# Optimization experiments

Hardware: AMD Instinct MI355X
Metric: run time of the kernel (lower is better)

The kernel has to match this reference:

```python
import jax, jax.numpy as jnp
import numpy as np

STATE = 24
ACT = 6
L1 = 100
L2 = 100
CHOL = ACT * (ACT + 1) // 2  # 21
BATCH = 262144


def setup_inputs() -> dict:
    key = jax.random.key(0)
    ks = jax.random.split(key, 9)
    return {
        "states": jax.random.normal(ks[0], (BATCH, STATE), jnp.float32),
        "W1": jax.random.normal(ks[1], (L1, STATE), jnp.float32) * (1.0 / np.sqrt(STATE)),
        "b1": jax.random.normal(ks[2], (L1,), jnp.float32) * 0.01,
        "W2": jax.random.normal(ks[3], (L2, L1), jnp.float32) * (1.0 / np.sqrt(L1)),
        "b2": jax.random.normal(ks[4], (L2,), jnp.float32) * 0.01,
        "Wm": jax.random.normal(ks[5], (ACT, L2), jnp.float32) * (1.0 / np.sqrt(L2)),
        "bm": jax.random.normal(ks[6], (ACT,), jnp.float32) * 0.01,
        "Wc": jax.random.normal(ks[7], (CHOL, L2), jnp.float32) * (1.0 / np.sqrt(L2)),
        "bc": jax.random.normal(ks[8], (CHOL,), jnp.float32) * 0.01,
    }


def reference(states, W1, b1, W2, b2, Wm, bm, Wc, bc):
    # 2-layer MLP backbone
    x = jax.nn.relu(states @ W1.T + b1)          # [B, L1]
    x = jax.nn.relu(x @ W2.T + b2)               # [B, L2]
    mean = jnp.tanh(x @ Wm.T + bm)               # [B, ACT]
    chol_vec = jax.nn.softplus(x @ Wc.T + bc)    # [B, CHOL]
    # Vectorized lower-triangular fill (replaces python double loop + .item()).
    # torch loop fills (i,j) with j<=i in row-major order == tril_indices order.
    rows, cols = jnp.tril_indices(ACT)
    chol = jnp.zeros((states.shape[0], ACT, ACT), chol_vec.dtype).at[:, rows, cols].set(chol_vec)
    return mean, chol
```

## Files before the change

kernel.cpp:

```cpp
#include <hip/hip_runtime.h>
#include <hip/hip_bf16.h>
#include <math.h>

typedef short bf16x8 __attribute__((ext_vector_type(8)));
typedef short bf16x4 __attribute__((ext_vector_type(4)));
typedef float f32x4 __attribute__((ext_vector_type(4)));

#define STATE 24
#define L1N 100

#define W1_STRIDE 40
#define K_STRIDE 136
#define W1_OFF 0
#define W2_OFF 4000
#define WH_OFF 17600
#define IMG_U32 10752
#define IMG_BYTES (IMG_U32 * 4)
#define IMG_HALVES (IMG_U32 * 2)

#define X_HALVES (32 * K_STRIDE)
#define NWAVES 4
#define LDS_BYTES (IMG_BYTES + NWAVES * X_HALVES * 2)

#define GRID 512

__device__ __constant__ int CHOFF[21] = {0,6,7,12,13,14,18,19,20,21,24,25,26,27,28,30,31,32,33,34,35};
__device__ __constant__ int ZOFF[15]  = {1,2,3,4,5,8,9,10,11,15,16,17,22,23,29};

__device__ inline unsigned short f2bf(float f) {
    union { float f; unsigned u; } v; v.f = f;
    unsigned r = v.u + 0x7FFFu + ((v.u >> 16) & 1u);
    return (unsigned short)(r >> 16);
}
__device__ inline unsigned pkbf(float lo, float hi) {
    __hip_bfloat162 h = __float22bfloat162_rn(float2{lo, hi});
    return *(const unsigned*)&h;
}
__device__ inline float fast_tanh(float x) {
    float e = __builtin_amdgcn_exp2f(x * 2.8853900817779268f);
    return 1.0f - 2.0f * __builtin_amdgcn_rcpf(e + 1.0f);
}
__device__ inline float fast_softplus(float v) {
    float u = __builtin_amdgcn_exp2f(fabsf(v) * -1.4426950408889634f);
    float l = __builtin_amdgcn_logf(1.0f + u) * 0.6931471805599453f;
    return fmaxf(v, 0.0f) + l;
}

__global__ __launch_bounds__(256) void prep_weights(
    const float* __restrict__ W1, const float* __restrict__ W2,
    const float* __restrict__ Wm, const float* __restrict__ Wc,
    unsigned* __restrict__ img)
{
    int i = blockIdx.x * 256 + threadIdx.x;
    if (i >= IMG_U32) return;
    float lo = 0.f, hi = 0.f;
    if (i < 2000) {
        int r = i / 20, k = (i % 20) * 2;
        if (k < STATE)     lo = W1[r * STATE + k];
        if (k + 1 < STATE) hi = W1[r * STATE + k + 1];
    } else if (i < 8800) {
        int j = i - 2000, r = j / 68, k = (j % 68) * 2;
        if (k < L1N)     lo = W2[r * L1N + k];
        if (k + 1 < L1N) hi = W2[r * L1N + k + 1];
    } else if (i < 10636) {
        int j = i - 8800, r = j / 68, k = (j % 68) * 2;
        const float* src = (r < 6) ? (Wm + r * L1N) : (Wc + (r - 6) * L1N);
        if (k < L1N)     lo = src[k];
        if (k + 1 < L1N) hi = src[k + 1];
    }
    img[i] = pkbf(lo, hi);
}

__global__ __launch_bounds__(256, 2) void actor_mfma(
    const float* __restrict__ states,
    const unsigned* __restrict__ img,
    const float* __restrict__ b1, const float* __restrict__ b2,
    const float* __restrict__ bm, const float* __restrict__ bc,
    float* __restrict__ out_mean, float* __restrict__ out_chol, int ntiles)
{
    extern __shared__ __align__(16) unsigned short smem[];
    const int tid = threadIdx.x;
    {
        const uint4* src = (const uint4*)img;
        uint4* dst = (uint4*)smem;
        for (int i = tid; i < IMG_BYTES / 16; i += 256) dst[i] = src[i];
    }
    const int wave = tid >> 6, lane = tid & 63, q = lane >> 4, c = lane & 15;
    unsigned short* W1s = smem + W1_OFF;
    unsigned short* W2s = smem + W2_OFF;
    unsigned short* Whs = smem + WH_OFF;
    unsigned short* X   = smem + IMG_HALVES + wave * X_HALVES;
    {
        unsigned* xz = (unsigned*)X;
        #pragma unroll
        for (int it = 0; it < 10; ++it) {
            int i = it * 64 + lane;
            int r = i / 20, s = i - r * 20;
            xz[r * 68 + 48 + s] = 0u;
        }
    }
    __syncthreads();

    f32x4 bias1[7], bias2[7];
    #pragma unroll
    for (int nt = 0; nt < 7; ++nt)
        #pragma unroll
        for (int i = 0; i < 4; ++i) {
            int f = nt * 16 + q * 4 + i; f = f < L1N ? f : L1N - 1;
            bias1[nt][i] = b1[f]; bias2[nt][i] = b2[f];
        }
    f32x4 bias3[2]; int eoff[8], ekind[8];
    #pragma unroll
    for (int ht = 0; ht < 2; ++ht)
        #pragma unroll
        for (int i = 0; i < 4; ++i) {
            int f = ht * 16 + q * 4 + i, e = ht * 4 + i;
            if (f < 6)       { bias3[ht][i] = bm[f];     eoff[e] = f;            ekind[e] = 0; }
            else if (f < 27) { bias3[ht][i] = bc[f - 6]; eoff[e] = CHOFF[f - 6]; ekind[e] = 1; }
            else             { bias3[ht][i] = 0.f;       eoff[e] = 0;            ekind[e] = -1; }
        }
    int zoff_[8], zrow_[8];
    #pragma unroll
    for (int it = 0; it < 8; ++it) {
        int idx = it * 64 + lane;
        int r = idx / 15;
        zrow_[it] = r; zoff_[it] = ZOFF[idx - r * 15 < 15 ? idx - r * 15 : 0];
    }

    float4 sv[4];
    auto loadStates = [&](int tt) {
        if (tt < ntiles && q < 3) {
            long rb = (long)tt * 128 + wave * 32;
            #pragma unroll
            for (int u = 0; u < 2; ++u) {
                const float* p = states + (rb + u * 16 + c) * STATE + q * 8;
                sv[u * 2]     = *(const float4*)p;
                sv[u * 2 + 1] = *(const float4*)(p + 4);
            }
        }
    };
    loadStates(blockIdx.x);

    for (int t = blockIdx.x; t < ntiles; t += GRID) {
        const long rowW = (long)t * 128 + wave * 32;

        union { bf16x8 v; unsigned u[4]; } sb[2];
        #pragma unroll
        for (int u = 0; u < 2; ++u) {
            if (q < 3) {
                sb[u].u[0] = pkbf(sv[u*2].x,   sv[u*2].y);
                sb[u].u[1] = pkbf(sv[u*2].z,   sv[u*2].w);
                sb[u].u[2] = pkbf(sv[u*2+1].x, sv[u*2+1].y);
                sb[u].u[3] = pkbf(sv[u*2+1].z, sv[u*2+1].w);
            } else sb[u].u[0] = sb[u].u[1] = sb[u].u[2] = sb[u].u[3] = 0u;
        }
        loadStates(t + GRID);

        #pragma unroll
        for (int nt = 0; nt < 7; ++nt) {
            int wr = nt * 16 + c; wr = wr < L1N ? wr : L1N - 1;
            bf16x8 wf = *(const bf16x8*)&W1s[wr * W1_STRIDE + q * 8];
            #pragma unroll
            for (int u = 0; u < 2; ++u) {
                f32x4 acc = bias1[nt];
                acc = __builtin_amdgcn_mfma_f32_16x16x32_bf16(wf, sb[u].v, acc, 0, 0, 0);
                if (nt * 16 + q * 4 < L1N) {
                    bf16x4 pk;
                    #pragma unroll
                    for (int i = 0; i < 4; ++i) pk[i] = (short)f2bf(fmaxf(acc[i], 0.f));
                    *(bf16x4*)&X[(u * 16 + c) * K_STRIDE + nt * 16 + q * 4] = pk;
                }
            }
        }

        bf16x8 ab[2][4];
        #pragma unroll
        for (int u = 0; u < 2; ++u)
            #pragma unroll
            for (int ks = 0; ks < 4; ++ks)
                ab[u][ks] = *(const bf16x8*)&X[(u * 16 + c) * K_STRIDE + ks * 32 + q * 8];
        f32x4 acc2[2][7];
        #pragma unroll
        for (int u = 0; u < 2; ++u)
            #pragma unroll
            for (int nt = 0; nt < 7; ++nt) acc2[u][nt] = bias2[nt];
        #pragma unroll
        for (int ks = 0; ks < 4; ++ks)
            #pragma unroll
            for (int nt = 0; nt < 7; ++nt) {
                int wr = nt * 16 + c; wr = wr < L1N ? wr : L1N - 1;
                bf16x8 wf = *(const bf16x8*)&W2s[wr * K_STRIDE + ks * 32 + q * 8];
                acc2[0][nt] = __builtin_amdgcn_mfma_f32_16x16x32_bf16(wf, ab[0][ks], acc2[0][nt], 0, 0, 0);
                acc2[1][nt] = __builtin_amdgcn_mfma_f32_16x16x32_bf16(wf, ab[1][ks], acc2[1][nt], 0, 0, 0);
            }
        #pragma unroll
        for (int nt = 0; nt < 7; ++nt)
            if (nt * 16 + q * 4 < L1N)
                #pragma unroll
                for (int u = 0; u < 2; ++u) {
                    bf16x4 pk;
                    #pragma unroll
                    for (int i = 0; i < 4; ++i) pk[i] = (short)f2bf(fmaxf(acc2[u][nt][i], 0.f));
                    *(bf16x4*)&X[(u * 16 + c) * K_STRIDE + nt * 16 + q * 4] = pk;
                }

        bf16x8 ab3[2][4];
        #pragma unroll
        for (int u = 0; u < 2; ++u)
            #pragma unroll
            for (int ks = 0; ks < 4; ++ks)
                ab3[u][ks] = *(const bf16x8*)&X[(u * 16 + c) * K_STRIDE + ks * 32 + q * 8];
        f32x4 acc3[2][2];
        #pragma unroll
        for (int u = 0; u < 2; ++u) { acc3[u][0] = bias3[0]; acc3[u][1] = bias3[1]; }
        #pragma unroll
        for (int ks = 0; ks < 4; ++ks)
            #pragma unroll
            for (int ht = 0; ht < 2; ++ht) {
                int wr = ht * 16 + c; wr = wr < 27 ? wr : 26;
                bf16x8 wf = *(const bf16x8*)&Whs[wr * K_STRIDE + ks * 32 + q * 8];
                acc3[0][ht] = __builtin_amdgcn_mfma_f32_16x16x32_bf16(wf, ab3[0][ks], acc3[0][ht], 0, 0, 0);
                acc3[1][ht] = __builtin_amdgcn_mfma_f32_16x16x32_bf16(wf, ab3[1][ks], acc3[1][ht], 0, 0, 0);
            }

        #pragma unroll
        for (int u = 0; u < 2; ++u) {
            const long r = rowW + u * 16 + c;
            float* mrow = out_mean + r * 6;
            float* crow = out_chol + r * 36;
            #pragma unroll
            for (int ht = 0; ht < 2; ++ht)
                #pragma unroll
                for (int i = 0; i < 4; ++i) {
                    int e = ht * 4 + i;
                    float v = acc3[u][ht][i];
                    if (ekind[e] == 0)      mrow[eoff[e]] = fast_tanh(v);
                    else if (ekind[e] == 1) crow[eoff[e]] = fast_softplus(v);
                }
        }
        #pragma unroll
        for (int it = 0; it < 8; ++it) {
            int idx = it * 64 + lane;
            if (idx < 480)
                out_chol[(rowW + zrow_[it]) * 36 + zoff_[it]] = 0.f;
        }
    }
}

extern "C" void kernel_launch(void* const* d_in, const int* in_sizes, int n_in,
                              void* d_out, int out_size, void* d_ws, size_t ws_size,
                              hipStream_t stream) {
    const float* states = (const float*)d_in[0];
    const float* W1 = (const float*)d_in[1];
    const float* b1 = (const float*)d_in[2];
    const float* W2 = (const float*)d_in[3];
    const float* b2 = (const float*)d_in[4];
    const float* Wm = (const float*)d_in[5];
    const float* bm = (const float*)d_in[6];
    const float* Wc = (const float*)d_in[7];
    const float* bc = (const float*)d_in[8];

    const int batch = in_sizes[0] / STATE;
    float* out_mean = (float*)d_out;
    float* out_chol = out_mean + (size_t)batch * 6;
    unsigned* img = (unsigned*)d_ws;

    hipFuncSetAttribute((const void*)actor_mfma,
                        hipFuncAttributeMaxDynamicSharedMemorySize, LDS_BYTES);

    prep_weights<<<(IMG_U32 + 255) / 256, 256, 0, stream>>>(W1, W2, Wm, Wc, img);
    const int ntiles = batch / 128;
    actor_mfma<<<GRID, 256, LDS_BYTES, stream>>>(states, img, b1, b2, bm, bc,
                                                 out_mean, out_chol, ntiles);
}
```

Measured before the change: 124.0 us.

## Fold biases into GEMMs, hold W1 in registers, stage coalesced output stores

Result: faster. 113.2 us (-8.6%).

```diff
diff --git a/kernel.cpp b/kernel.cpp
--- a/kernel.cpp
+++ b/kernel.cpp
@@ -9,20 +9,18 @@
 #define STATE 24
 #define L1N 100
 
+#define IMG_W2_U32 2000
+#define IMG_U32 10752
 #define W1_STRIDE 40
 #define K_STRIDE 136
-#define W1_OFF 0
-#define W2_OFF 4000
-#define WH_OFF 17600
-#define IMG_U32 10752
-#define IMG_BYTES (IMG_U32 * 4)
-#define IMG_HALVES (IMG_U32 * 2)
-
-#define X_HALVES (32 * K_STRIDE)
-#define NWAVES 4
-#define LDS_BYTES (IMG_BYTES + NWAVES * X_HALVES * 2)
-
-#define GRID 512
+
+#define W2_HALVES 13600
+#define WH_HALVES 3672
+#define X_OFF (W2_HALVES + WH_HALVES)
+#define X_HALVES (16 * K_STRIDE)
+#define LDS_HALVES (X_OFF + 4 * X_HALVES)
+#define LDS_BYTES (LDS_HALVES * 2)
+#define GRID 768
 
 __device__ __constant__ int CHOFF[21] = {0,6,7,12,13,14,18,19,20,21,24,25,26,27,28,30,31,32,33,34,35};
 __device__ __constant__ int ZOFF[15]  = {1,2,3,4,5,8,9,10,11,15,16,17,22,23,29};
@@ -47,8 +45,10 @@
 }
 
 __global__ __launch_bounds__(256) void prep_weights(
-    const float* __restrict__ W1, const float* __restrict__ W2,
-    const float* __restrict__ Wm, const float* __restrict__ Wc,
+    const float* __restrict__ W1, const float* __restrict__ b1,
+    const float* __restrict__ W2, const float* __restrict__ b2,
+    const float* __restrict__ Wm, const float* __restrict__ bm,
+    const float* __restrict__ Wc, const float* __restrict__ bc,
     unsigned* __restrict__ img)
 {
     int i = blockIdx.x * 256 + threadIdx.x;
@@ -56,193 +56,170 @@
     float lo = 0.f, hi = 0.f;
     if (i < 2000) {
         int r = i / 20, k = (i % 20) * 2;
-        if (k < STATE)     lo = W1[r * STATE + k];
-        if (k + 1 < STATE) hi = W1[r * STATE + k + 1];
+        if (k < STATE)      { lo = W1[r * STATE + k]; hi = W1[r * STATE + k + 1]; }
+        else if (k == STATE)  lo = b1[r];
     } else if (i < 8800) {
         int j = i - 2000, r = j / 68, k = (j % 68) * 2;
-        if (k < L1N)     lo = W2[r * L1N + k];
-        if (k + 1 < L1N) hi = W2[r * L1N + k + 1];
+        if (k < L1N)      { lo = W2[r * L1N + k]; hi = (k + 1 < L1N) ? W2[r * L1N + k + 1] : 0.f; }
+        else if (k == L1N)  lo = b2[r];
     } else if (i < 10636) {
         int j = i - 8800, r = j / 68, k = (j % 68) * 2;
-        const float* src = (r < 6) ? (Wm + r * L1N) : (Wc + (r - 6) * L1N);
-        if (k < L1N)     lo = src[k];
-        if (k + 1 < L1N) hi = src[k + 1];
+        const float* src; float bias;
+        if (r < 6) { src = Wm + r * L1N; bias = bm[r]; }
+        else       { src = Wc + (r - 6) * L1N; bias = bc[r - 6]; }
+        if (k < L1N)      { lo = src[k]; hi = (k + 1 < L1N) ? src[k + 1] : 0.f; }
+        else if (k == L1N)  lo = bias;
     }
     img[i] = pkbf(lo, hi);
 }
 
-__global__ __launch_bounds__(256, 2) void actor_mfma(
+__global__ __launch_bounds__(256, 3) void actor_mfma(
     const float* __restrict__ states,
     const unsigned* __restrict__ img,
-    const float* __restrict__ b1, const float* __restrict__ b2,
-    const float* __restrict__ bm, const float* __restrict__ bc,
     float* __restrict__ out_mean, float* __restrict__ out_chol, int ntiles)
 {
     extern __shared__ __align__(16) unsigned short smem[];
     const int tid = threadIdx.x;
     {
-        const uint4* src = (const uint4*)img;
+        const uint4* src = (const uint4*)(img + IMG_W2_U32);
         uint4* dst = (uint4*)smem;
-        for (int i = tid; i < IMG_BYTES / 16; i += 256) dst[i] = src[i];
+        for (int i = tid; i < (IMG_U32 - IMG_W2_U32) / 4; i += 256) dst[i] = src[i];
     }
     const int wave = tid >> 6, lane = tid & 63, q = lane >> 4, c = lane & 15;
-    unsigned short* W1s = smem + W1_OFF;
-    unsigned short* W2s = smem + W2_OFF;
-    unsigned short* Whs = smem + WH_OFF;
-    unsigned short* X   = smem + IMG_HALVES + wave * X_HALVES;
-    {
-        unsigned* xz = (unsigned*)X;
-        #pragma unroll
-        for (int it = 0; it < 10; ++it) {
-            int i = it * 64 + lane;
-            int r = i / 20, s = i - r * 20;
-            xz[r * 68 + 48 + s] = 0u;
-        }
-    }
+    unsigned short* W2s = smem;
+    unsigned short* Whs = smem + W2_HALVES;
+    unsigned short* X   = smem + X_OFF + wave * X_HALVES;
+    unsigned* Xw  = (unsigned*)X;
+    float* stage  = (float*)X;
+
+    bf16x8 wf1[7];
+    #pragma unroll
+    for (int nt = 0; nt < 7; ++nt) {
+        int wr = nt * 16 + c; wr = wr < L1N ? wr : L1N - 1;
+        wf1[nt] = *(const bf16x8*)((const unsigned short*)img + wr * W1_STRIDE + q * 8);
+    }
+
     __syncthreads();
 
-    f32x4 bias1[7], bias2[7];
-    #pragma unroll
-    for (int nt = 0; nt < 7; ++nt)
-        #pragma unroll
-        for (int i = 0; i < 4; ++i) {
-            int f = nt * 16 + q * 4 + i; f = f < L1N ? f : L1N - 1;
-            bias1[nt][i] = b1[f]; bias2[nt][i] = b2[f];
-        }
-    f32x4 bias3[2]; int eoff[8], ekind[8];
+    #pragma unroll
+    for (int it = 0; it < 5; ++it) {
+        int idx = it * 64 + lane;
+        if (idx < 288) {
+            int r = idx / 18, s = idx - r * 18;
+            Xw[r * 68 + 50 + s] = (s == 0) ? 0x00003F80u : 0u;
+        }
+    }
+
+    int scol[8], skind[8];
     #pragma unroll
     for (int ht = 0; ht < 2; ++ht)
         #pragma unroll
         for (int i = 0; i < 4; ++i) {
             int f = ht * 16 + q * 4 + i, e = ht * 4 + i;
-            if (f < 6)       { bias3[ht][i] = bm[f];     eoff[e] = f;            ekind[e] = 0; }
-            else if (f < 27) { bias3[ht][i] = bc[f - 6]; eoff[e] = CHOFF[f - 6]; ekind[e] = 1; }
-            else             { bias3[ht][i] = 0.f;       eoff[e] = 0;            ekind[e] = -1; }
-        }
-    int zoff_[8], zrow_[8];
-    #pragma unroll
-    for (int it = 0; it < 8; ++it) {
-        int idx = it * 64 + lane;
-        int r = idx / 15;
-        zrow_[it] = r; zoff_[it] = ZOFF[idx - r * 15 < 15 ? idx - r * 15 : 0];
-    }
-
-    float4 sv[4];
+            if (f < 6)       { scol[e] = 36 + f;        skind[e] = 0; }
+            else if (f < 27) { scol[e] = CHOFF[f - 6];  skind[e] = 1; }
+            else             { scol[e] = 0;             skind[e] = -1; }
+        }
+    int zcol[4];
+    const int nz = (q == 3) ? 3 : 4;
+    #pragma unroll
+    for (int z = 0; z < 4; ++z) zcol[z] = ZOFF[(q * 4 + z) < 15 ? (q * 4 + z) : 14];
+
+    float4 sv[2];
     auto loadStates = [&](int tt) {
         if (tt < ntiles && q < 3) {
-            long rb = (long)tt * 128 + wave * 32;
-            #pragma unroll
-            for (int u = 0; u < 2; ++u) {
-                const float* p = states + (rb + u * 16 + c) * STATE + q * 8;
-                sv[u * 2]     = *(const float4*)p;
-                sv[u * 2 + 1] = *(const float4*)(p + 4);
-            }
+            const float* p = states + ((long)tt * 64 + wave * 16 + c) * STATE + q * 8;
+            sv[0] = *(const float4*)p;
+            sv[1] = *(const float4*)(p + 4);
         }
     };
     loadStates(blockIdx.x);
 
     for (int t = blockIdx.x; t < ntiles; t += GRID) {
-        const long rowW = (long)t * 128 + wave * 32;
-
-        union { bf16x8 v; unsigned u[4]; } sb[2];
-        #pragma unroll
-        for (int u = 0; u < 2; ++u) {
-            if (q < 3) {
-                sb[u].u[0] = pkbf(sv[u*2].x,   sv[u*2].y);
-                sb[u].u[1] = pkbf(sv[u*2].z,   sv[u*2].w);
-                sb[u].u[2] = pkbf(sv[u*2+1].x, sv[u*2+1].y);
-                sb[u].u[3] = pkbf(sv[u*2+1].z, sv[u*2+1].w);
-            } else sb[u].u[0] = sb[u].u[1] = sb[u].u[2] = sb[u].u[3] = 0u;
+        const long rowW = (long)t * 64 + wave * 16;
+
+        union { bf16x8 v; unsigned u[4]; } sb;
+        if (q < 3) {
+            sb.u[0] = pkbf(sv[0].x, sv[0].y); sb.u[1] = pkbf(sv[0].z, sv[0].w);
+            sb.u[2] = pkbf(sv[1].x, sv[1].y); sb.u[3] = pkbf(sv[1].z, sv[1].w);
+        } else {
+            sb.u[0] = 0x00003F80u; sb.u[1] = sb.u[2] = sb.u[3] = 0u;
         }
         loadStates(t + GRID);
 
         #pragma unroll
         for (int nt = 0; nt < 7; ++nt) {
-            int wr = nt * 16 + c; wr = wr < L1N ? wr : L1N - 1;
-            bf16x8 wf = *(const bf16x8*)&W1s[wr * W1_STRIDE + q * 8];
-            #pragma unroll
-            for (int u = 0; u < 2; ++u) {
-                f32x4 acc = bias1[nt];
-                acc = __builtin_amdgcn_mfma_f32_16x16x32_bf16(wf, sb[u].v, acc, 0, 0, 0);
-                if (nt * 16 + q * 4 < L1N) {
-                    bf16x4 pk;
-                    #pragma unroll
-                    for (int i = 0; i < 4; ++i) pk[i] = (short)f2bf(fmaxf(acc[i], 0.f));
-                    *(bf16x4*)&X[(u * 16 + c) * K_STRIDE + nt * 16 + q * 4] = pk;
-                }
-            }
-        }
-
-        bf16x8 ab[2][4];
-        #pragma unroll
-        for (int u = 0; u < 2; ++u)
-            #pragma unroll
-            for (int ks = 0; ks < 4; ++ks)
-                ab[u][ks] = *(const bf16x8*)&X[(u * 16 + c) * K_STRIDE + ks * 32 + q * 8];
-        f32x4 acc2[2][7];
-        #pragma unroll
-        for (int u = 0; u < 2; ++u)
-            #pragma unroll
-            for (int nt = 0; nt < 7; ++nt) acc2[u][nt] = bias2[nt];
+            f32x4 acc = {0.f, 0.f, 0.f, 0.f};
+            acc = __builtin_amdgcn_mfma_f32_16x16x32_bf16(wf1[nt], sb.v, acc, 0, 0, 0);
+            if (nt * 16 + q * 4 < L1N) {
+                bf16x4 pk;
+                #pragma unroll
+                for (int i = 0; i < 4; ++i) pk[i] = (short)f2bf(fmaxf(acc[i], 0.f));
+                *(bf16x4*)&X[c * K_STRIDE + nt * 16 + q * 4] = pk;
+            }
+        }
+
+        bf16x8 ab[4];
+        #pragma unroll
+        for (int ks = 0; ks < 4; ++ks)
+            ab[ks] = *(const bf16x8*)&X[c * K_STRIDE + ks * 32 + q * 8];
+        f32x4 acc2[7];
+        #pragma unroll
+        for (int nt = 0; nt < 7; ++nt) acc2[nt] = (f32x4){0.f, 0.f, 0.f, 0.f};
         #pragma unroll
         for (int ks = 0; ks < 4; ++ks)
             #pragma unroll
             for (int nt = 0; nt < 7; ++nt) {
                 int wr = nt * 16 + c; wr = wr < L1N ? wr : L1N - 1;
                 bf16x8 wf = *(const bf16x8*)&W2s[wr * K_STRIDE + ks * 32 + q * 8];
-                acc2[0][nt] = __builtin_amdgcn_mfma_f32_16x16x32_bf16(wf, ab[0][ks], acc2[0][nt], 0, 0, 0);
-                acc2[1][nt] = __builtin_amdgcn_mfma_f32_16x16x32_bf16(wf, ab[1][ks], acc2[1][nt], 0, 0, 0);
+                acc2[nt] = __builtin_amdgcn_mfma_f32_16x16x32_bf16(wf, ab[ks], acc2[nt], 0, 0, 0);
             }
         #pragma unroll
         for (int nt = 0; nt < 7; ++nt)
-            if (nt * 16 + q * 4 < L1N)
+            if (nt * 16 + q * 4 < L1N) {
+                bf16x4 pk;
                 #pragma unroll
-                for (int u = 0; u < 2; ++u) {
-                    bf16x4 pk;
-                    #pragma unroll
-                    for (int i = 0; i < 4; ++i) pk[i] = (short)f2bf(fmaxf(acc2[u][nt][i], 0.f));
-                    *(bf16x4*)&X[(u * 16 + c) * K_STRIDE + nt * 16 + q * 4] = pk;
-                }
-
-        bf16x8 ab3[2][4];
-        #pragma unroll
-        for (int u = 0; u < 2; ++u)
-            #pragma unroll
-            for (int ks = 0; ks < 4; ++ks)
-                ab3[u][ks] = *(const bf16x8*)&X[(u * 16 + c) * K_STRIDE + ks * 32 + q * 8];
-        f32x4 acc3[2][2];
-        #pragma unroll
-        for (int u = 0; u < 2; ++u) { acc3[u][0] = bias3[0]; acc3[u][1] = bias3[1]; }
+                for (int i = 0; i < 4; ++i) pk[i] = (short)f2bf(fmaxf(acc2[nt][i], 0.f));
+                *(bf16x4*)&X[c * K_STRIDE + nt * 16 + q * 4] = pk;
+            }
+
+        bf16x8 ab3[4];
+        #pragma unroll
+        for (int ks = 0; ks < 4; ++ks)
+            ab3[ks] = *(const bf16x8*)&X[c * K_STRIDE + ks * 32 + q * 8];
+        f32x4 acc3[2];
+        acc3[0] = (f32x4){0.f, 0.f, 0.f, 0.f};
+        acc3[1] = (f32x4){0.f, 0.f, 0.f, 0.f};
         #pragma unroll
         for (int ks = 0; ks < 4; ++ks)
             #pragma unroll
             for (int ht = 0; ht < 2; ++ht) {
                 int wr = ht * 16 + c; wr = wr < 27 ? wr : 26;
                 bf16x8 wf = *(const bf16x8*)&Whs[wr * K_STRIDE + ks * 32 + q * 8];
-                acc3[0][ht] = __builtin_amdgcn_mfma_f32_16x16x32_bf16(wf, ab3[0][ks], acc3[0][ht], 0, 0, 0);
-                acc3[1][ht] = __builtin_amdgcn_mfma_f32_16x16x32_bf16(wf, ab3[1][ks], acc3[1][ht], 0, 0, 0);
-            }
-
-        #pragma unroll
-        for (int u = 0; u < 2; ++u) {
-            const long r = rowW + u * 16 + c;
-            float* mrow = out_mean + r * 6;
-            float* crow = out_chol + r * 36;
-            #pragma unroll
-            for (int ht = 0; ht < 2; ++ht)
-                #pragma unroll
-                for (int i = 0; i < 4; ++i) {
-                    int e = ht * 4 + i;
-                    float v = acc3[u][ht][i];
-                    if (ekind[e] == 0)      mrow[eoff[e]] = fast_tanh(v);
-                    else if (ekind[e] == 1) crow[eoff[e]] = fast_softplus(v);
-                }
-        }
-        #pragma unroll
-        for (int it = 0; it < 8; ++it) {
-            int idx = it * 64 + lane;
-            if (idx < 480)
-                out_chol[(rowW + zrow_[it]) * 36 + zoff_[it]] = 0.f;
+                acc3[ht] = __builtin_amdgcn_mfma_f32_16x16x32_bf16(wf, ab3[ks], acc3[ht], 0, 0, 0);
+            }
+
+        #pragma unroll
+        for (int e = 0; e < 8; ++e) {
+            float v = acc3[e >> 2][e & 3];
+            if (skind[e] == 0)      stage[c * 68 + scol[e]] = fast_tanh(v);
+            else if (skind[e] == 1) stage[c * 68 + scol[e]] = fast_softplus(v);
+        }
+        #pragma unroll
+        for (int z = 0; z < 4; ++z)
+            if (z < nz) stage[c * 68 + zcol[z]] = 0.f;
+
+        if (lane < 48) {
+            float2 m = *(const float2*)&stage[(lane / 3) * 68 + 36 + (lane % 3) * 2];
+            *(float2*)(out_mean + rowW * 6 + lane * 2) = m;
+        }
+        #pragma unroll
+        for (int it = 0; it < 3; ++it) {
+            int j = it * 64 + lane;
+            if (j < 144) {
+                float4 v = *(const float4*)&stage[(j / 9) * 68 + (j % 9) * 4];
+                *(float4*)(out_chol + rowW * 36 + j * 4) = v;
+            }
         }
     }
 }
@@ -268,8 +245,8 @@
     hipFuncSetAttribute((const void*)actor_mfma,
                         hipFuncAttributeMaxDynamicSharedMemorySize, LDS_BYTES);
 
-    prep_weights<<<(IMG_U32 + 255) / 256, 256, 0, stream>>>(W1, W2, Wm, Wc, img);
-    const int ntiles = batch / 128;
-    actor_mfma<<<GRID, 256, LDS_BYTES, stream>>>(states, img, b1, b2, bm, bc,
-                                                 out_mean, out_chol, ntiles);
-}
+    prep_weights<<<(IMG_U32 + 255) / 256, 256, 0, stream>>>(W1, b1, W2, b2,
+                                                            Wm, bm, Wc, bc, img);
+    const int ntiles = batch / 64;
+    actor_mfma<<<GRID, 256, LDS_BYTES, stream>>>(states, img, out_mean, out_chol, ntiles);
+}
```
